# Kernel tuning notes

Measured on AMD Instinct MI355X. Metric: run time of the kernel, lower is better.

The kernel has to match this reference:

```python
import jax, jax.numpy as jnp
import numpy as np

VOCAB = 32000
EMB = 256
UNITS = 1024


def setup_inputs() -> dict:
    key = jax.random.key(0)
    ks = jax.random.split(key, 6)
    B, S = 128, 256
    x = jax.random.randint(ks[0], (B, S), 0, VOCAB, dtype=jnp.int32)
    hidden = jnp.zeros((B, UNITS), jnp.float32)
    # Parameters (Keras GRU v2, reset_after=True): kernel W [EMB, 3*UNITS],
    # recurrent kernel U [UNITS, 3*UNITS], bias b [2, 3*UNITS] (input bias, recurrent bias)
    emb = jax.random.normal(ks[1], (VOCAB, EMB), jnp.float32) * 0.05
    W = jax.random.normal(ks[2], (EMB, 3 * UNITS), jnp.float32) * (1.0 / np.sqrt(EMB))
    U = jax.random.normal(ks[3], (UNITS, 3 * UNITS), jnp.float32) * (1.0 / np.sqrt(UNITS))
    b = jnp.zeros((2, 3 * UNITS), jnp.float32)
    return {"x": x, "hidden": hidden, "emb": emb, "W": W, "U": U, "b": b}


def _gru_seq(xp, hidden, U, b_rec):
    # xp: [S, B, 3H] precomputed input projections (incl. input bias)
    H = hidden.shape[-1]

    def step(h, xt):
        rec = h @ U + b_rec                       # [B, 3H]
        xz, xr, xh = xt[:, :H], xt[:, H:2 * H], xt[:, 2 * H:]
        rz, rr, rh = rec[:, :H], rec[:, H:2 * H], rec[:, 2 * H:]
        z = jax.nn.sigmoid(xz + rz)
        r = jax.nn.sigmoid(xr + rr)
        hh = jnp.tanh(xh + r * rh)                # reset_after=True
        h_new = z * h + (1.0 - z) * hh
        return h_new, h_new

    state, outs = jax.lax.scan(step, hidden, xp)
    return outs, state


def reference(x, hidden, emb, W, U, b):
    xe = emb[x]                                   # [B, S, EMB]
    # Precompute all input-side projections in one big GEMM
    xp = jnp.einsum('bse,eh->bsh', xe, W) + b[0]  # [B, S, 3H]
    xp = jnp.swapaxes(xp, 0, 1)                   # [S, B, 3H]
    outs, state = _gru_seq(xp, hidden, U, b[1])
    output = jnp.swapaxes(outs, 0, 1)             # [B, S, H]
    return output, state
```

## Files before the change

kernel.cpp:

```cpp
#include <hip/hip_runtime.h>

#define B_   128
#define S_   256
#define EMB_ 256
#define H_   1024
#define NH3  3072

#define MG      16
#define HS      16
#define THREADS 768

typedef _Float16 f16;
typedef _Float16 h8 __attribute__((ext_vector_type(8)));
typedef float    f4 __attribute__((ext_vector_type(4)));
typedef unsigned long long u64;

#define AL64(pp) __hip_atomic_load((pp), __ATOMIC_RELAXED, __HIP_MEMORY_SCOPE_AGENT)

__global__ void gather_kernel(const int* __restrict__ x, const float* __restrict__ emb,
                              f16* __restrict__ xe16) {
  int m = blockIdx.x, k = threadIdx.x;
  int b = m & 127, s = m >> 7;
  int row = x[b * S_ + s];
  xe16[m * EMB_ + k] = (f16)emb[row * EMB_ + k];
}

__global__ void transpose_cvt(const float* __restrict__ in, f16* __restrict__ out,
                              int K, int N) {
  __shared__ float tile[32][33];
  int n0 = blockIdx.x * 32, k0 = blockIdx.y * 32;
  int tx = threadIdx.x & 31, ty = threadIdx.x >> 5;
#pragma unroll
  for (int i = 0; i < 4; ++i)
    tile[ty + 8 * i][tx] = in[(k0 + ty + 8 * i) * N + n0 + tx];
  __syncthreads();
#pragma unroll
  for (int i = 0; i < 4; ++i)
    out[(n0 + ty + 8 * i) * K + k0 + tx] = (f16)tile[tx][ty + 8 * i];
}

__launch_bounds__(THREADS, 3)
__global__ void gru_kernel(const f16* __restrict__ xe16, const f16* __restrict__ Ut,
                           const f16* __restrict__ Wt, const float* __restrict__ hidden,
                           const float* __restrict__ bvec, float* __restrict__ out,
                           f16* __restrict__ h16, int* __restrict__ flags) {
  __shared__ f16   h_lds[2][MG * H_];
  __shared__ f16   xe_lds[2][MG * EMB_];
  __shared__ float recS[4][MG][68];

  const int tid = threadIdx.x;
  const int bid = blockIdx.x;
  const int p   = bid & 3;
  const int w   = bid >> 2;
  const int hc0 = w * HS;
  const int rowA = p * 32, rowB = p * 32 + 16;

  const int lane = tid & 63;
  const int wv   = tid >> 6;
  const int ksp  = wv & 3;
  const int cp   = wv >> 2;
  const int ln   = lane & 15;
  const int klo  = lane >> 4;
  const int bl   = tid >> 4;
  const int jl   = tid & 15;

  int* flA = flags + p * 128;
  int* flB = flags + p * 128 + 64;

  h8 uf[8]; h8 wf[2];
  {
    const f16* u0 = Ut + (size_t)(cp * H_ + hc0 + ln) * H_ + ksp * 256 + klo * 8;
#pragma unroll
    for (int kt = 0; kt < 8; ++kt) uf[kt] = *(const h8*)(u0 + kt * 32);
    const f16* w0 = Wt + (size_t)(cp * H_ + hc0 + ln) * EMB_ + ksp * 64 + klo * 8;
    wf[0] = *(const h8*)(w0);
    wf[1] = *(const h8*)(w0 + 32);
  }
#pragma unroll
  for (int kt = 0; kt < 8; ++kt) asm volatile("" : "+v"(uf[kt]));
  asm volatile("" : "+v"(wf[0]), "+v"(wf[1]));

  float hprevA = 0.f, hprevB = 0.f, bz = 0.f, brr = 0.f, bxh = 0.f, brh = 0.f;
  size_t obaseA = 0, obaseB = 0, soffA = 0, soffB = 0;
  if (tid < 256) {
    int col = hc0 + jl;
    bz  = bvec[col] + bvec[NH3 + col];
    brr = bvec[H_ + col] + bvec[NH3 + H_ + col];
    bxh = bvec[2 * H_ + col];
    brh = bvec[NH3 + 2 * H_ + col];
    hprevA = hidden[(size_t)(rowA + bl) * H_ + col];
    hprevB = hidden[(size_t)(rowB + bl) * H_ + col];
    obaseA = ((size_t)(rowA + bl) * S_) * H_ + col;
    obaseB = ((size_t)(rowB + bl) * S_) * H_ + col;
    soffA  = (size_t)(rowA + bl) * H_ + col;
    soffB  = (size_t)(rowB + bl) * H_ + col;
  }

  for (int idx = tid; idx < 2 * MG * H_ / 4; idx += THREADS) {
    int grp = idx >> 12, i = idx & 4095;
    int r = i >> 8, c4 = i & 255;
    float4 hv = ((const float4*)(hidden + (size_t)(p * 32 + grp * 16 + r) * H_))[c4];
    unsigned lo = ((unsigned)__builtin_bit_cast(unsigned short, (f16)hv.y) << 16)
                |  (unsigned)__builtin_bit_cast(unsigned short, (f16)hv.x);
    unsigned hi = ((unsigned)__builtin_bit_cast(unsigned short, (f16)hv.w) << 16)
                |  (unsigned)__builtin_bit_cast(unsigned short, (f16)hv.z);
    uint2 pk = {lo, hi};
    *(uint2*)((char*)h_lds[grp] + r * 2048 + ((c4 * 8) ^ ((r & 7) << 4))) = pk;
  }
  for (int idx = tid; idx < 2 * MG * EMB_ / 8; idx += THREADS) {
    int grp = idx >> 9, i = idx & 511;
    int r = i >> 5, c = i & 31;
    uint4 v = ((const uint4*)(xe16 + (size_t)(p * 32 + grp * 16) * EMB_))[i];
    *(uint4*)((char*)xe_lds[grp] + r * 512 + ((c * 16) ^ ((r & 7) << 4))) = v;
  }
  __syncthreads();

#define MFMA_PHASE(GRP)                                                          \
  {                                                                              \
    f4 aU = {0.f,0.f,0.f,0.f}, aW = {0.f,0.f,0.f,0.f};                           \
    const char* hb = (const char*)h_lds[GRP] + ln * 2048;                        \
    const char* xb = (const char*)xe_lds[GRP] + ln * 512;                        \
    const int rm = (ln & 7) << 4;                                                \
    _Pragma("unroll")                                                            \
    for (int kt = 0; kt < 8; ++kt) {                                             \
      h8 a = *(const h8*)(hb + ((ksp * 512 + kt * 64 + klo * 16) ^ rm));         \
      aU = __builtin_amdgcn_mfma_f32_16x16x32_f16(a, uf[kt], aU, 0, 0, 0);       \
    }                                                                            \
    _Pragma("unroll")                                                            \
    for (int kt = 0; kt < 2; ++kt) {                                             \
      h8 a = *(const h8*)(xb + ((ksp * 128 + kt * 64 + klo * 16) ^ rm));         \
      aW = __builtin_amdgcn_mfma_f32_16x16x32_f16(a, wf[kt], aW, 0, 0, 0);       \
    }                                                                            \
    _Pragma("unroll")                                                            \
    for (int j = 0; j < 4; ++j) {                                                \
      int r = klo * 4 + j;                                                       \
      if (cp == 0)      recS[ksp][r][ln]      = aU[j] + aW[j];                   \
      else if (cp == 1) recS[ksp][r][16 + ln] = aU[j] + aW[j];                   \
      else { recS[ksp][r][32 + ln] = aW[j]; recS[ksp][r][48 + ln] = aU[j]; }     \
    }                                                                            \
  }

#define GATES(hprev, outv)                                                       \
  {                                                                              \
    float az = recS[0][bl][jl] + recS[1][bl][jl] + recS[2][bl][jl]               \
             + recS[3][bl][jl] + bz;                                             \
    float ar = recS[0][bl][16+jl] + recS[1][bl][16+jl] + recS[2][bl][16+jl]      \
             + recS[3][bl][16+jl] + brr;                                         \
    float xh = recS[0][bl][32+jl] + recS[1][bl][32+jl] + recS[2][bl][32+jl]      \
             + recS[3][bl][32+jl] + bxh;                                         \
    float rhu = recS[0][bl][48+jl] + recS[1][bl][48+jl] + recS[2][bl][48+jl]     \
              + recS[3][bl][48+jl] + brh;                                        \
    float z  = 1.f / (1.f + __expf(-az));                                        \
    float r  = 1.f / (1.f + __expf(-ar));                                        \
    float hh = 1.f - 2.f / (1.f + __expf(2.f * (xh + r * rhu)));                 \
    float hn = z * hprev + (1.f - z) * hh;                                       \
    hprev = hn; outv = hn;                                                       \
  }

#define PULL(GRP, rowbase, buf, FL, NEED)                                        \
  {                                                                              \
    for (;;) {                                                                   \
      int f = AL64((FL) + lane);                                                 \
      if (__all(f >= (NEED))) break;                                             \
      __builtin_amdgcn_s_sleep(1);                                               \
    }                                                                            \
    const u64* src = (const u64*)(h16 + (size_t)(buf) * (B_ * H_)                \
                                  + (size_t)(rowbase) * H_);                     \
    u64 v0 = AL64(src + tid);        u64 v1 = AL64(src + tid + 768);             \
    u64 v2 = AL64(src + tid + 1536); u64 v3 = AL64(src + tid + 2304);            \
    u64 v4 = AL64(src + tid + 3072); u64 v5 = 0;                                 \
    if (tid < 256) v5 = AL64(src + 3840 + tid);                                  \
    { int i_ = tid;        int r_ = i_ >> 8, c_ = i_ & 255;                      \
      *(u64*)((char*)h_lds[GRP] + r_ * 2048 + ((c_ * 8) ^ ((r_ & 7) << 4))) = v0; } \
    { int i_ = tid + 768;  int r_ = i_ >> 8, c_ = i_ & 255;                      \
      *(u64*)((char*)h_lds[GRP] + r_ * 2048 + ((c_ * 8) ^ ((r_ & 7) << 4))) = v1; } \
    { int i_ = tid + 1536; int r_ = i_ >> 8, c_ = i_ & 255;                      \
      *(u64*)((char*)h_lds[GRP] + r_ * 2048 + ((c_ * 8) ^ ((r_ & 7) << 4))) = v2; } \
    { int i_ = tid + 2304; int r_ = i_ >> 8, c_ = i_ & 255;                      \
      *(u64*)((char*)h_lds[GRP] + r_ * 2048 + ((c_ * 8) ^ ((r_ & 7) << 4))) = v3; } \
    { int i_ = tid + 3072; int r_ = i_ >> 8, c_ = i_ & 255;                      \
      *(u64*)((char*)h_lds[GRP] + r_ * 2048 + ((c_ * 8) ^ ((r_ & 7) << 4))) = v4; } \
    if (tid < 256) { int i_ = 3840 + tid; int r_ = i_ >> 8, c_ = i_ & 255;       \
      *(u64*)((char*)h_lds[GRP] + r_ * 2048 + ((c_ * 8) ^ ((r_ & 7) << 4))) = v5; } \
  }

#define XE_STAGE(GRP, rowbase)                                                   \
  {                                                                              \
    const uint4* xs = (const uint4*)(xe16 + ((size_t)(t + 1) * B_ + (rowbase)) * EMB_); \
    char* dst = (char*)xe_lds[GRP];                                              \
    int i0 = (tid - 512) * 2;                                                    \
    uint4 x0 = xs[i0], x1 = xs[i0 + 1];                                          \
    { int r_ = i0 >> 5, c_ = i0 & 31;                                            \
      *(uint4*)(dst + r_ * 512 + ((c_ * 16) ^ ((r_ & 7) << 4))) = x0; }          \
    { int i1 = i0 + 1; int r_ = i1 >> 5, c_ = i1 & 31;                           \
      *(uint4*)(dst + r_ * 512 + ((c_ * 16) ^ ((r_ & 7) << 4))) = x1; }          \
  }

  for (int t = 0; t < S_; ++t) {
    const int nb = (t + 1) & 1;
    MFMA_PHASE(0)
    __syncthreads();
    if (tid < 256) {
      float outvA;
      GATES(hprevA, outvA)
      if (t < S_ - 1) {
        unsigned short hb16 = __builtin_bit_cast(unsigned short, (f16)outvA);
        __hip_atomic_store((unsigned short*)h16 + (size_t)nb * (B_ * H_) + soffA,
                           hb16, __ATOMIC_RELAXED, __HIP_MEMORY_SCOPE_AGENT);
      }
      out[obaseA + (size_t)t * H_] = outvA;
      if (t == S_ - 1) out[(size_t)B_ * S_ * H_ + soffA] = outvA;
    } else if (tid >= 512 && t < S_ - 1) {
      XE_STAGE(0, rowA)
    }
    if (t > 0) PULL(1, rowB, t & 1, flB, t)
    asm volatile("s_waitcnt vmcnt(0)" ::: "memory");
    __syncthreads();
    if (t < S_ - 1 && tid == 0)
      __hip_atomic_store(&flA[w], t + 1, __ATOMIC_RELAXED, __HIP_MEMORY_SCOPE_AGENT);
    MFMA_PHASE(1)
    __syncthreads();
    if (tid < 256) {
      float outvB;
      GATES(hprevB, outvB)
      if (t < S_ - 1) {
        unsigned short hb16 = __builtin_bit_cast(unsigned short, (f16)outvB);
        __hip_atomic_store((unsigned short*)h16 + (size_t)nb * (B_ * H_) + soffB,
                           hb16, __ATOMIC_RELAXED, __HIP_MEMORY_SCOPE_AGENT);
      }
      out[obaseB + (size_t)t * H_] = outvB;
      if (t == S_ - 1) out[(size_t)B_ * S_ * H_ + soffB] = outvB;
    } else if (tid >= 512 && t < S_ - 1) {
      XE_STAGE(1, rowB)
    }
    if (t < S_ - 1) {
      PULL(0, rowA, nb, flA, t + 1)
      asm volatile("s_waitcnt vmcnt(0)" ::: "memory");
      __syncthreads();
      if (tid == 0)
        __hip_atomic_store(&flB[w], t + 1, __ATOMIC_RELAXED, __HIP_MEMORY_SCOPE_AGENT);
    }
  }
}

extern "C" void kernel_launch(void* const* d_in, const int* in_sizes, int n_in,
                              void* d_out, int out_size, void* d_ws, size_t ws_size,
                              hipStream_t stream) {
  const int*   x      = (const int*)  d_in[0];
  const float* hidden = (const float*)d_in[1];
  const float* emb    = (const float*)d_in[2];
  const float* W      = (const float*)d_in[3];
  const float* U      = (const float*)d_in[4];
  const float* bvec   = (const float*)d_in[5];
  float* out = (float*)d_out;

  char* ws = (char*)d_ws;
  f16* Ut    = (f16*)(ws);
  f16* Wt    = (f16*)(ws + 6291456);
  f16* xe16  = (f16*)(ws + 7864320);
  f16* h16   = (f16*)(ws + 24641536);
  int* flags = (int*)(ws + 25165824);

  hipMemsetAsync(flags, 0, 2048, stream);
  hipLaunchKernelGGL(transpose_cvt, dim3(NH3 / 32, H_ / 32), dim3(256), 0, stream,
                     U, Ut, H_, NH3);
  hipLaunchKernelGGL(transpose_cvt, dim3(NH3 / 32, EMB_ / 32), dim3(256), 0, stream,
                     W, Wt, EMB_, NH3);
  hipLaunchKernelGGL(gather_kernel, dim3(B_ * S_), dim3(EMB_), 0, stream, x, emb, xe16);

  void* args[] = { (void*)&xe16, (void*)&Ut, (void*)&Wt, (void*)&hidden,
                   (void*)&bvec, (void*)&out, (void*)&h16, (void*)&flags };
  hipLaunchCooperativeKernel(reinterpret_cast<void*>(gru_kernel),
                             dim3(256), dim3(THREADS), args, 0, stream);
}
```

Baseline: 1.058 ms.

## Specialize warps and overlap h-state pulls with MFMA phases in GRU recurrence

Reorganizes the per-timestep schedule of the persistent GRU kernel into three thread roles. Threads 0-255 compute gates, threads 256-703 poll flags and issue the global loads of the other group's hidden state before the MFMA phase, and threads 704-767 stage the embedding tiles. The pulled values stay in registers across the MFMA work and are written to LDS afterwards, and the output stores are moved after the flag publish. The aim is to hide cross-block hidden-state latency behind compute, at the cost of more registers and an extra barrier per step.

```diff
diff --git a/kernel.cpp b/kernel.cpp
--- a/kernel.cpp
+++ b/kernel.cpp
@@ -16,6 +16,7 @@
 typedef unsigned long long u64;
 
 #define AL64(pp) __hip_atomic_load((pp), __ATOMIC_RELAXED, __HIP_MEMORY_SCOPE_AGENT)
+#define ALI(pp)  __hip_atomic_load((pp), __ATOMIC_RELAXED, __HIP_MEMORY_SCOPE_AGENT)
 
 __global__ void gather_kernel(const int* __restrict__ x, const float* __restrict__ emb,
                               f16* __restrict__ xe16) {
@@ -157,89 +158,103 @@
     hprev = hn; outv = hn;                                                       \
   }
 
-#define PULL(GRP, rowbase, buf, FL, NEED)                                        \
-  {                                                                              \
-    for (;;) {                                                                   \
-      int f = AL64((FL) + lane);                                                 \
-      if (__all(f >= (NEED))) break;                                             \
-      __builtin_amdgcn_s_sleep(1);                                               \
-    }                                                                            \
-    const u64* src = (const u64*)(h16 + (size_t)(buf) * (B_ * H_)                \
+#define POLLW(FL, NEED)                                                          \
+  for (;;) { int f = ALI((FL) + lane); if (__all(f >= (NEED))) break;            \
+             __builtin_amdgcn_s_sleep(1); }
+
+#define PULL_ISSUE(rowbase, buf, V)                                              \
+  { const u64* src = (const u64*)(h16 + (size_t)(buf) * (B_ * H_)                \
                                   + (size_t)(rowbase) * H_);                     \
-    u64 v0 = AL64(src + tid);        u64 v1 = AL64(src + tid + 768);             \
-    u64 v2 = AL64(src + tid + 1536); u64 v3 = AL64(src + tid + 2304);            \
-    u64 v4 = AL64(src + tid + 3072); u64 v5 = 0;                                 \
-    if (tid < 256) v5 = AL64(src + 3840 + tid);                                  \
-    { int i_ = tid;        int r_ = i_ >> 8, c_ = i_ & 255;                      \
-      *(u64*)((char*)h_lds[GRP] + r_ * 2048 + ((c_ * 8) ^ ((r_ & 7) << 4))) = v0; } \
-    { int i_ = tid + 768;  int r_ = i_ >> 8, c_ = i_ & 255;                      \
-      *(u64*)((char*)h_lds[GRP] + r_ * 2048 + ((c_ * 8) ^ ((r_ & 7) << 4))) = v1; } \
-    { int i_ = tid + 1536; int r_ = i_ >> 8, c_ = i_ & 255;                      \
-      *(u64*)((char*)h_lds[GRP] + r_ * 2048 + ((c_ * 8) ^ ((r_ & 7) << 4))) = v2; } \
-    { int i_ = tid + 2304; int r_ = i_ >> 8, c_ = i_ & 255;                      \
-      *(u64*)((char*)h_lds[GRP] + r_ * 2048 + ((c_ * 8) ^ ((r_ & 7) << 4))) = v3; } \
-    { int i_ = tid + 3072; int r_ = i_ >> 8, c_ = i_ & 255;                      \
-      *(u64*)((char*)h_lds[GRP] + r_ * 2048 + ((c_ * 8) ^ ((r_ & 7) << 4))) = v4; } \
-    if (tid < 256) { int i_ = 3840 + tid; int r_ = i_ >> 8, c_ = i_ & 255;       \
-      *(u64*)((char*)h_lds[GRP] + r_ * 2048 + ((c_ * 8) ^ ((r_ & 7) << 4))) = v5; } \
-  }
-
-#define XE_STAGE(GRP, rowbase)                                                   \
-  {                                                                              \
-    const uint4* xs = (const uint4*)(xe16 + ((size_t)(t + 1) * B_ + (rowbase)) * EMB_); \
-    char* dst = (char*)xe_lds[GRP];                                              \
-    int i0 = (tid - 512) * 2;                                                    \
-    uint4 x0 = xs[i0], x1 = xs[i0 + 1];                                          \
-    { int r_ = i0 >> 5, c_ = i0 & 31;                                            \
-      *(uint4*)(dst + r_ * 512 + ((c_ * 16) ^ ((r_ & 7) << 4))) = x0; }          \
-    { int i1 = i0 + 1; int r_ = i1 >> 5, c_ = i1 & 31;                           \
-      *(uint4*)(dst + r_ * 512 + ((c_ * 16) ^ ((r_ & 7) << 4))) = x1; }          \
-  }
+    int tp = tid - 256;                                                          \
+    _Pragma("unroll")                                                            \
+    for (int k = 0; k < 9; ++k) V[k] = AL64(src + tp + k * 448);                 \
+    if (tp < 64) V[9] = AL64(src + 4032 + tp); }
+
+#define PULL_LDS(GRP, V)                                                         \
+  { int tp = tid - 256;                                                          \
+    _Pragma("unroll")                                                            \
+    for (int k = 0; k < 9; ++k) {                                                \
+      int idx = tp + k * 448; int r_ = idx >> 8, c_ = idx & 255;                 \
+      *(u64*)((char*)h_lds[GRP] + r_ * 2048 + ((c_ * 8) ^ ((r_ & 7) << 4))) = V[k]; } \
+    if (tp < 64) { int idx = 4032 + tp; int r_ = idx >> 8, c_ = idx & 255;       \
+      *(u64*)((char*)h_lds[GRP] + r_ * 2048 + ((c_ * 8) ^ ((r_ & 7) << 4))) = V[9]; } }
+
+#define XE_STAGE11(GRP, rowbase, tt)                                             \
+  { const uint4* xs = (const uint4*)(xe16 + ((size_t)(tt) * B_ + (rowbase)) * EMB_); \
+    char* dst = (char*)xe_lds[GRP]; int tq = tid - 704;                          \
+    _Pragma("unroll")                                                            \
+    for (int i = 0; i < 8; ++i) {                                                \
+      int idx = tq + i * 64; uint4 v = xs[idx];                                  \
+      int r_ = idx >> 5, c_ = idx & 31;                                          \
+      *(uint4*)(dst + r_ * 512 + ((c_ * 16) ^ ((r_ & 7) << 4))) = v; } }
 
   for (int t = 0; t < S_; ++t) {
     const int nb = (t + 1) & 1;
+    u64 V[10];
+    float outvA = 0.f, outvB = 0.f;
+
+    if (t > 0 && tid >= 256 && tid < 704) {
+      POLLW(flB, t)
+      PULL_ISSUE(rowB, t & 1, V)
+    }
     MFMA_PHASE(0)
     __syncthreads();
     if (tid < 256) {
-      float outvA;
       GATES(hprevA, outvA)
       if (t < S_ - 1) {
         unsigned short hb16 = __builtin_bit_cast(unsigned short, (f16)outvA);
         __hip_atomic_store((unsigned short*)h16 + (size_t)nb * (B_ * H_) + soffA,
                            hb16, __ATOMIC_RELAXED, __HIP_MEMORY_SCOPE_AGENT);
       }
-      out[obaseA + (size_t)t * H_] = outvA;
-      if (t == S_ - 1) out[(size_t)B_ * S_ * H_ + soffA] = outvA;
-    } else if (tid >= 512 && t < S_ - 1) {
-      XE_STAGE(0, rowA)
-    }
-    if (t > 0) PULL(1, rowB, t & 1, flB, t)
-    asm volatile("s_waitcnt vmcnt(0)" ::: "memory");
+      asm volatile("s_waitcnt vmcnt(0)" ::: "memory");
+    } else if (tid < 704) {
+      if (t > 0) {
+        asm volatile("s_waitcnt vmcnt(0)" ::: "memory");
+        PULL_LDS(1, V)
+      }
+    } else {
+      if (t < S_ - 1) XE_STAGE11(0, rowA, t + 1)
+    }
     __syncthreads();
     if (t < S_ - 1 && tid == 0)
       __hip_atomic_store(&flA[w], t + 1, __ATOMIC_RELAXED, __HIP_MEMORY_SCOPE_AGENT);
+
     MFMA_PHASE(1)
     __syncthreads();
     if (tid < 256) {
-      float outvB;
       GATES(hprevB, outvB)
       if (t < S_ - 1) {
         unsigned short hb16 = __builtin_bit_cast(unsigned short, (f16)outvB);
         __hip_atomic_store((unsigned short*)h16 + (size_t)nb * (B_ * H_) + soffB,
                            hb16, __ATOMIC_RELAXED, __HIP_MEMORY_SCOPE_AGENT);
       }
+      asm volatile("s_waitcnt vmcnt(0)" ::: "memory");
+    } else if (tid < 704) {
+      if (t < S_ - 1) {
+        POLLW(flA, t + 1)
+        PULL_ISSUE(rowA, nb, V)
+      }
+    } else {
+      if (t < S_ - 1) XE_STAGE11(1, rowB, t + 1)
+    }
+    __syncthreads();
+    if (t < S_ - 1 && tid == 0)
+      __hip_atomic_store(&flB[w], t + 1, __ATOMIC_RELAXED, __HIP_MEMORY_SCOPE_AGENT);
+
+    if (tid < 256) {
+      out[obaseA + (size_t)t * H_] = outvA;
       out[obaseB + (size_t)t * H_] = outvB;
-      if (t == S_ - 1) out[(size_t)B_ * S_ * H_ + soffB] = outvB;
-    } else if (tid >= 512 && t < S_ - 1) {
-      XE_STAGE(1, rowB)
-    }
-    if (t < S_ - 1) {
-      PULL(0, rowA, nb, flA, t + 1)
-      asm volatile("s_waitcnt vmcnt(0)" ::: "memory");
-      __syncthreads();
-      if (tid == 0)
-        __hip_atomic_store(&flB[w], t + 1, __ATOMIC_RELAXED, __HIP_MEMORY_SCOPE_AGENT);
-    }
+      if (t == S_ - 1) {
+        out[(size_t)B_ * S_ * H_ + soffA] = outvA;
+        out[(size_t)B_ * S_ * H_ + soffB] = outvB;
+      }
+    } else if (tid < 704) {
+      if (t < S_ - 1) {
+        asm volatile("s_waitcnt vmcnt(0)" ::: "memory");
+        PULL_LDS(0, V)
+      }
+    }
+    __syncthreads();
   }
 }
 
```

Result: slower. 1.864 ms (+76.2%).
